# Kernel tuning notes

Measured on AMD Instinct MI355X. Metric: run time of the kernel, lower is better.

The kernel has to match this reference:

```python
import jax, jax.numpy as jnp
import numpy as np

# cfg constants (from init_kwargs)
RBF_START = 0.0
RBF_END = 10.0
RBF_STEPS = 32
ENERGY_SCALE = 1.0
EPS = 1e-10

L, R, E, F, P = 64, 4096, 32, 64, 8


def setup_inputs() -> dict:
    key = jax.random.key(0)
    ks = jax.random.split(key, 6)
    return {
        "lig_feat": jax.random.normal(ks[0], (L, E, F), dtype=jnp.float32),
        "rec_feat": jax.random.normal(ks[1], (R, E, F), dtype=jnp.float32),
        "lig_coords": jax.random.normal(ks[2], (P, L, 3), dtype=jnp.float32),
        "rec_coord": jax.random.normal(ks[3], (R, 3), dtype=jnp.float32),
        "weight": jax.random.normal(ks[4], (), dtype=jnp.float32),
        "bias": jax.random.normal(ks[5], (), dtype=jnp.float32),
    }


def reference(lig_feat, rec_feat, lig_coords, rec_coord, weight, bias):
    # attention coefficients: [L, R, E]
    atn = jnp.einsum('lef,ref->lre', lig_feat, rec_feat)
    mu = jnp.linspace(RBF_START, RBF_END, RBF_STEPS, dtype=jnp.float32)  # [E]
    sigma = (RBF_START - RBF_END) / RBF_STEPS

    def energy(lig_coord):  # lig_coord: [L, 3]
        # cdist_diff: eps added per-coordinate before sum, as in the torch code
        diff = lig_coord[:, None, :] - rec_coord[None, :, :]      # [L, R, 3]
        dists = jnp.sqrt(((diff * diff) + EPS).sum(-1))            # [L, R]
        z = (dists[..., None] - mu) / sigma                        # [L, R, E]
        rbfs = jnp.exp(-(z * z))
        return (atn * rbfs * ENERGY_SCALE).sum()

    Us = jax.vmap(energy)(lig_coords)  # [P]
    # ScaleOutput
    return Us * weight + bias
```

## Files before the change

### kernel.cpp

```cpp
#include <hip/hip_runtime.h>

#define NL 64
#define NR 4096
#define NE 32
#define NF 64
#define NP 8

#define DSCALE 3.8435917081166390f
#define MUSTEP 1.2398683f
#define EPS3   3e-10f

typedef _Float16 f16x8 __attribute__((ext_vector_type(8)));
typedef __fp16   h16x2 __attribute__((ext_vector_type(2)));
typedef float    f32x4 __attribute__((ext_vector_type(4)));

#define NBLK 1024

#define COORD_B 0
#define DTAB_B  8192
#define REC_B   24576

__global__ __launch_bounds__(256, 4)
void ff_main(const float* __restrict__ lig_feat,
             const float* __restrict__ rec_feat,
             const float* __restrict__ lig_coords,
             const float* __restrict__ rec_coord,
             float* __restrict__ ws)
{
    __shared__ __align__(16) char smem[40960];

    const int t    = threadIdx.x;
    const int bid  = blockIdx.x;
    const int rb   = bid & 255;
    const int eb   = bid >> 8;
    const int r0   = rb * 16;
    const int e0   = eb * 8;
    const int lane = t & 63;
    const int wv   = t >> 6;
    const int l0   = wv * 16;
    const int cn   = lane & 15;
    const int kg   = lane >> 4;

#pragma unroll
    for (int j = 0; j < 6; ++j) {
        const int s = j * 256 + t;
        const int p = s / 192;
        const int rem = s - p * 192;
        const int l = rem / 3, c = rem - l * 3;
        *(float*)(smem + COORD_B + (l * 8 + p) * 16 + c * 4) = lig_coords[s];
    }
    const int srow = t >> 4, sfq = t & 15;
    const int rswz = (8 * sfq) ^ ((srow & 7) << 4);
#pragma unroll
    for (int e = 0; e < 8; ++e) {
        const float4 v = *(const float4*)&rec_feat[((r0 + srow) * NE + e0 + e) * NF + sfq * 4];
        union { h16x2 h[2]; uint2 u; } pk;
        pk.h[0] = __builtin_amdgcn_cvt_pkrtz(v.x, v.y);
        pk.h[1] = __builtin_amdgcn_cvt_pkrtz(v.z, v.w);
        *(uint2*)(smem + REC_B + e * 2048 + srow * 128 + rswz) = pk.u;
    }
    __syncthreads();

    {
        const int bl = t >> 2;
        const int br = t & 3;
        float4 lp[NP];
#pragma unroll
        for (int p = 0; p < NP; ++p)
            lp[p] = *(const float4*)(smem + COORD_B + (bl * 8 + p) * 16);
#pragma unroll
        for (int j = 0; j < 4; ++j) {
            const int r = br + 4 * j;
            const float rx = rec_coord[(r0 + r) * 3 + 0];
            const float ry = rec_coord[(r0 + r) * 3 + 1];
            const float rz = rec_coord[(r0 + r) * 3 + 2];
            float d[NP];
#pragma unroll
            for (int p = 0; p < NP; ++p) {
                const float dx = lp[p].x - rx, dy = lp[p].y - ry, dz = lp[p].z - rz;
                const float d2 = fmaf(dx, dx, fmaf(dy, dy, fmaf(dz, dz, EPS3)));
                d[p] = __builtin_amdgcn_sqrtf(d2) * DSCALE;
            }
            union { h16x2 h[4]; uint4 u; } pk;
#pragma unroll
            for (int q = 0; q < 4; ++q)
                pk.h[q] = __builtin_amdgcn_cvt_pkrtz(d[2 * q], d[2 * q + 1]);
            *(uint4*)(smem + DTAB_B + bl * 256 + ((r * 16) ^ ((bl & 7) * 16))) = pk.u;
        }
    }
    __syncthreads();

    float ds[4][NP];
#pragma unroll
    for (int reg = 0; reg < 4; ++reg) {
        const int l = l0 + kg * 4 + reg;
        union { uint4 u; _Float16 h[8]; } pk;
        pk.u = *(const uint4*)(smem + DTAB_B + l * 256 + ((cn * 16) ^ ((l & 7) * 16)));
#pragma unroll
        for (int p = 0; p < NP; ++p) ds[reg][p] = (float)pk.h[p];
    }

    const int bsw = (cn & 7) << 4;
    const int b0o = REC_B + cn * 128 + ((kg * 16) ^ bsw);
    const int b1o = REC_B + cn * 128 + ((kg * 16 + 64) ^ bsw);
    const float* ligb = &lig_feat[((l0 + cn) * NE + e0) * NF + kg * 8];

    float U[NP];
#pragma unroll
    for (int p = 0; p < NP; ++p) U[p] = 0.f;

#pragma unroll
    for (int ee = 0; ee < 8; ++ee) {
        const float4 af0 = *(const float4*)(ligb + ee * NF + 0);
        const float4 af1 = *(const float4*)(ligb + ee * NF + 4);
        const float4 af2 = *(const float4*)(ligb + ee * NF + 32);
        const float4 af3 = *(const float4*)(ligb + ee * NF + 36);
        union { h16x2 h[4]; f16x8 v; } a0, a1;
        a0.h[0] = __builtin_amdgcn_cvt_pkrtz(af0.x, af0.y);
        a0.h[1] = __builtin_amdgcn_cvt_pkrtz(af0.z, af0.w);
        a0.h[2] = __builtin_amdgcn_cvt_pkrtz(af1.x, af1.y);
        a0.h[3] = __builtin_amdgcn_cvt_pkrtz(af1.z, af1.w);
        a1.h[0] = __builtin_amdgcn_cvt_pkrtz(af2.x, af2.y);
        a1.h[1] = __builtin_amdgcn_cvt_pkrtz(af2.z, af2.w);
        a1.h[2] = __builtin_amdgcn_cvt_pkrtz(af3.x, af3.y);
        a1.h[3] = __builtin_amdgcn_cvt_pkrtz(af3.z, af3.w);
        const f16x8 b0 = *(const f16x8*)(smem + b0o + ee * 2048);
        const f16x8 b1 = *(const f16x8*)(smem + b1o + ee * 2048);
        f32x4 C = {0.f, 0.f, 0.f, 0.f};
        C = __builtin_amdgcn_mfma_f32_16x16x32_f16(a0.v, b0, C, 0, 0, 0);
        C = __builtin_amdgcn_mfma_f32_16x16x32_f16(a1.v, b1, C, 0, 0, 0);

        const float mu = (float)(e0 + ee) * MUSTEP;
#pragma unroll
        for (int reg = 0; reg < 4; ++reg) {
            const float a = C[reg];
#pragma unroll
            for (int p = 0; p < NP; ++p) {
                const float z = ds[reg][p] - mu;
                U[p] = fmaf(a, __builtin_amdgcn_exp2f(-(z * z)), U[p]);
            }
        }
    }

#pragma unroll
    for (int p = 0; p < NP; ++p) {
        float v = U[p];
        for (int off = 32; off; off >>= 1) v += __shfl_down(v, off, 64);
        U[p] = v;
    }
    float* wred = (float*)(smem + COORD_B);
    if (lane == 0) {
#pragma unroll
        for (int p = 0; p < NP; ++p) wred[wv * 8 + p] = U[p];
    }
    __syncthreads();
    if (t < NP)
        ws[t * NBLK + bid] = wred[t] + wred[8 + t] + wred[16 + t] + wred[24 + t];
}

__global__ __launch_bounds__(512)
void ff_fin(const float* __restrict__ ws,
            const float* __restrict__ w,
            const float* __restrict__ b,
            float* __restrict__ out) {
    const int t = threadIdx.x, lane = t & 63, p = t >> 6;
    float s = 0.f;
#pragma unroll
    for (int j = 0; j < NBLK / 256; ++j) {
        const float4 v = *(const float4*)&ws[p * NBLK + j * 256 + lane * 4];
        s += (v.x + v.y) + (v.z + v.w);
    }
    for (int off = 32; off; off >>= 1) s += __shfl_down(s, off, 64);
    if (lane == 0) out[p] = fmaf(s, w[0], b[0]);
}

extern "C" void kernel_launch(void* const* d_in, const int* in_sizes, int n_in,
                              void* d_out, int out_size, void* d_ws, size_t ws_size,
                              hipStream_t stream) {
    const float* lig_feat   = (const float*)d_in[0];
    const float* rec_feat   = (const float*)d_in[1];
    const float* lig_coords = (const float*)d_in[2];
    const float* rec_coord  = (const float*)d_in[3];
    const float* weight     = (const float*)d_in[4];
    const float* bias       = (const float*)d_in[5];
    float* out = (float*)d_out;
    float* ws  = (float*)d_ws;

    hipLaunchKernelGGL(ff_main, dim3(NBLK), dim3(256), 0, stream,
                       lig_feat, rec_feat, lig_coords, rec_coord, ws);
    hipLaunchKernelGGL(ff_fin, dim3(1), dim3(512), 0, stream,
                       ws, weight, bias, out);
}
```

Before: 29.41 us.

## Load receptor features directly from global and compute distances per lane

Stops staging receptor features through shared memory and instead has each lane load its MFMA B operand straight from global memory, converting to fp16 in registers. The shared fp16 distance table is also removed: each lane now computes the 32 distances it needs from padded shared ligand coordinates. This drops one barrier and most of the LDS footprint, which may allow higher occupancy. In exchange it adds redundant global loads of rec_feat, since the four waves each fetch the same data, and it recomputes sqrt per lane.

```diff
diff --git a/kernel.cpp b/kernel.cpp
--- a/kernel.cpp
+++ b/kernel.cpp
@@ -16,9 +16,8 @@
 
 #define NBLK 1024
 
-#define COORD_B 0
-#define DTAB_B  8192
-#define REC_B   24576
+#define CSTRIDE 144
+#define WRED_B  (NL * CSTRIDE)
 
 __global__ __launch_bounds__(256, 4)
 void ff_main(const float* __restrict__ lig_feat,
@@ -27,7 +26,7 @@
              const float* __restrict__ rec_coord,
              float* __restrict__ ws)
 {
-    __shared__ __align__(16) char smem[40960];
+    __shared__ __align__(16) char smem[WRED_B + 128];
 
     const int t    = threadIdx.x;
     const int bid  = blockIdx.x;
@@ -47,63 +46,29 @@
         const int p = s / 192;
         const int rem = s - p * 192;
         const int l = rem / 3, c = rem - l * 3;
-        *(float*)(smem + COORD_B + (l * 8 + p) * 16 + c * 4) = lig_coords[s];
-    }
-    const int srow = t >> 4, sfq = t & 15;
-    const int rswz = (8 * sfq) ^ ((srow & 7) << 4);
-#pragma unroll
-    for (int e = 0; e < 8; ++e) {
-        const float4 v = *(const float4*)&rec_feat[((r0 + srow) * NE + e0 + e) * NF + sfq * 4];
-        union { h16x2 h[2]; uint2 u; } pk;
-        pk.h[0] = __builtin_amdgcn_cvt_pkrtz(v.x, v.y);
-        pk.h[1] = __builtin_amdgcn_cvt_pkrtz(v.z, v.w);
-        *(uint2*)(smem + REC_B + e * 2048 + srow * 128 + rswz) = pk.u;
+        *(float*)(smem + l * CSTRIDE + p * 16 + c * 4) = lig_coords[s];
     }
     __syncthreads();
 
-    {
-        const int bl = t >> 2;
-        const int br = t & 3;
-        float4 lp[NP];
-#pragma unroll
-        for (int p = 0; p < NP; ++p)
-            lp[p] = *(const float4*)(smem + COORD_B + (bl * 8 + p) * 16);
-#pragma unroll
-        for (int j = 0; j < 4; ++j) {
-            const int r = br + 4 * j;
-            const float rx = rec_coord[(r0 + r) * 3 + 0];
-            const float ry = rec_coord[(r0 + r) * 3 + 1];
-            const float rz = rec_coord[(r0 + r) * 3 + 2];
-            float d[NP];
-#pragma unroll
-            for (int p = 0; p < NP; ++p) {
-                const float dx = lp[p].x - rx, dy = lp[p].y - ry, dz = lp[p].z - rz;
-                const float d2 = fmaf(dx, dx, fmaf(dy, dy, fmaf(dz, dz, EPS3)));
-                d[p] = __builtin_amdgcn_sqrtf(d2) * DSCALE;
-            }
-            union { h16x2 h[4]; uint4 u; } pk;
-#pragma unroll
-            for (int q = 0; q < 4; ++q)
-                pk.h[q] = __builtin_amdgcn_cvt_pkrtz(d[2 * q], d[2 * q + 1]);
-            *(uint4*)(smem + DTAB_B + bl * 256 + ((r * 16) ^ ((bl & 7) * 16))) = pk.u;
-        }
-    }
-    __syncthreads();
-
+    const int rr = r0 + cn;
+    const float rx = rec_coord[rr * 3 + 0];
+    const float ry = rec_coord[rr * 3 + 1];
+    const float rz = rec_coord[rr * 3 + 2];
     float ds[4][NP];
 #pragma unroll
     for (int reg = 0; reg < 4; ++reg) {
         const int l = l0 + kg * 4 + reg;
-        union { uint4 u; _Float16 h[8]; } pk;
-        pk.u = *(const uint4*)(smem + DTAB_B + l * 256 + ((cn * 16) ^ ((l & 7) * 16)));
 #pragma unroll
-        for (int p = 0; p < NP; ++p) ds[reg][p] = (float)pk.h[p];
+        for (int p = 0; p < NP; ++p) {
+            const float4 lc = *(const float4*)(smem + l * CSTRIDE + p * 16);
+            const float dx = lc.x - rx, dy = lc.y - ry, dz = lc.z - rz;
+            const float d2 = fmaf(dx, dx, fmaf(dy, dy, fmaf(dz, dz, EPS3)));
+            ds[reg][p] = __builtin_amdgcn_sqrtf(d2) * DSCALE;
+        }
     }
 
-    const int bsw = (cn & 7) << 4;
-    const int b0o = REC_B + cn * 128 + ((kg * 16) ^ bsw);
-    const int b1o = REC_B + cn * 128 + ((kg * 16 + 64) ^ bsw);
     const float* ligb = &lig_feat[((l0 + cn) * NE + e0) * NF + kg * 8];
+    const float* recb = &rec_feat[((r0 + cn) * NE + e0) * NF + kg * 8];
 
     float U[NP];
 #pragma unroll
@@ -115,7 +80,11 @@
         const float4 af1 = *(const float4*)(ligb + ee * NF + 4);
         const float4 af2 = *(const float4*)(ligb + ee * NF + 32);
         const float4 af3 = *(const float4*)(ligb + ee * NF + 36);
-        union { h16x2 h[4]; f16x8 v; } a0, a1;
+        const float4 bf0 = *(const float4*)(recb + ee * NF + 0);
+        const float4 bf1 = *(const float4*)(recb + ee * NF + 4);
+        const float4 bf2 = *(const float4*)(recb + ee * NF + 32);
+        const float4 bf3 = *(const float4*)(recb + ee * NF + 36);
+        union { h16x2 h[4]; f16x8 v; } a0, a1, b0, b1;
         a0.h[0] = __builtin_amdgcn_cvt_pkrtz(af0.x, af0.y);
         a0.h[1] = __builtin_amdgcn_cvt_pkrtz(af0.z, af0.w);
         a0.h[2] = __builtin_amdgcn_cvt_pkrtz(af1.x, af1.y);
@@ -124,11 +93,17 @@
         a1.h[1] = __builtin_amdgcn_cvt_pkrtz(af2.z, af2.w);
         a1.h[2] = __builtin_amdgcn_cvt_pkrtz(af3.x, af3.y);
         a1.h[3] = __builtin_amdgcn_cvt_pkrtz(af3.z, af3.w);
-        const f16x8 b0 = *(const f16x8*)(smem + b0o + ee * 2048);
-        const f16x8 b1 = *(const f16x8*)(smem + b1o + ee * 2048);
+        b0.h[0] = __builtin_amdgcn_cvt_pkrtz(bf0.x, bf0.y);
+        b0.h[1] = __builtin_amdgcn_cvt_pkrtz(bf0.z, bf0.w);
+        b0.h[2] = __builtin_amdgcn_cvt_pkrtz(bf1.x, bf1.y);
+        b0.h[3] = __builtin_amdgcn_cvt_pkrtz(bf1.z, bf1.w);
+        b1.h[0] = __builtin_amdgcn_cvt_pkrtz(bf2.x, bf2.y);
+        b1.h[1] = __builtin_amdgcn_cvt_pkrtz(bf2.z, bf2.w);
+        b1.h[2] = __builtin_amdgcn_cvt_pkrtz(bf3.x, bf3.y);
+        b1.h[3] = __builtin_amdgcn_cvt_pkrtz(bf3.z, bf3.w);
         f32x4 C = {0.f, 0.f, 0.f, 0.f};
-        C = __builtin_amdgcn_mfma_f32_16x16x32_f16(a0.v, b0, C, 0, 0, 0);
-        C = __builtin_amdgcn_mfma_f32_16x16x32_f16(a1.v, b1, C, 0, 0, 0);
+        C = __builtin_amdgcn_mfma_f32_16x16x32_f16(a0.v, b0.v, C, 0, 0, 0);
+        C = __builtin_amdgcn_mfma_f32_16x16x32_f16(a1.v, b1.v, C, 0, 0, 0);
 
         const float mu = (float)(e0 + ee) * MUSTEP;
 #pragma unroll
@@ -148,7 +123,7 @@
         for (int off = 32; off; off >>= 1) v += __shfl_down(v, off, 64);
         U[p] = v;
     }
-    float* wred = (float*)(smem + COORD_B);
+    float* wred = (float*)(smem + WRED_B);
     if (lane == 0) {
 #pragma unroll
         for (int p = 0; p < NP; ++p) wred[wv * 8 + p] = U[p];
```

Result: slower. 45.18 us (+53.6%).
